# Kernel tuning notes

Hardware: AMD Instinct MI355X
Metric: run time of the kernel (lower is better)

The kernel has to match this reference:

```python
import jax, jax.numpy as jnp
import numpy as np

N_FEAT = 1024
NEG_INF = -1e30  # stand-in for -inf that is safe in fp32 softmax


def setup_inputs() -> dict:
    key = jax.random.key(0)
    k1, k2 = jax.random.split(key)
    T, C = 4096, N_FEAT
    x = jax.random.normal(k1, (T, C), dtype=jnp.float32)
    W = jax.random.normal(k2, (C, 3 * C), dtype=jnp.float32) * (1.0 / np.sqrt(C))
    b = jnp.zeros((3 * C,), dtype=jnp.float32)
    return {"x": x, "W": W, "b": b, "n_padd": 0}


def reference(x, W, b, n_padd):
    T, C = x.shape
    qkv = x @ W + b                      # [T, 3C]
    q, k, v = jnp.split(qkv, 3, axis=1)  # each [T, C]
    att = (q @ k.T) * (1.0 / jnp.sqrt(jnp.float32(C)))  # [T, T]
    idx = jnp.arange(T)
    # causal mask AND padding mask: only keys >= n_padd for queries >= n_padd
    mask = (idx[None, :] <= idx[:, None]) & (idx[None, :] >= n_padd) & (idx[:, None] >= n_padd)
    att = jnp.where(mask, att, NEG_INF)
    att = jax.nn.softmax(att, axis=-1)
    y = att @ v                          # [T, C]
    return y
```

## Files before the change

kernel.cpp:

```cpp
#include <hip/hip_runtime.h>
#include <hip/hip_bf16.h>
#include <math.h>

#define C_DIM 1024
#define QKS  2048

typedef __attribute__((ext_vector_type(8))) short bf16x8;
typedef __attribute__((ext_vector_type(4))) float f32x4;

__device__ __forceinline__ unsigned short f2bf(float f) {
  __hip_bfloat16 h = __float2bfloat16(f);
  return *(reinterpret_cast<unsigned short*>(&h));
}
__device__ __forceinline__ float bf2f(unsigned short u) {
  return __uint_as_float(((unsigned int)u) << 16);
}
__device__ __forceinline__ f32x4 mfma16(bf16x8 a, bf16x8 b, f32x4 c) {
  return __builtin_amdgcn_mfma_f32_16x16x32_bf16(a, b, c, 0, 0, 0);
}
__device__ __forceinline__ void gload_lds16(const unsigned short* g,
                                            unsigned short* l) {
  __builtin_amdgcn_global_load_lds(
      (const __attribute__((address_space(1))) void*)(g),
      (__attribute__((address_space(3))) void*)(l), 16, 0, 0);
}

#define VMCNT(n)  asm volatile("s_waitcnt vmcnt(" #n ")" ::: "memory")
#define LGKMCNT0  asm volatile("s_waitcnt lgkmcnt(0)" ::: "memory")
#define SBAR      __builtin_amdgcn_sched_barrier(0)
#define BARRIER   __builtin_amdgcn_s_barrier()
#define PRIO1     __builtin_amdgcn_s_setprio(1)
#define PRIO0     __builtin_amdgcn_s_setprio(0)

__global__ __launch_bounds__(256) void cast_x(
    const float* __restrict__ x, unsigned short* __restrict__ xb) {
  const int i = (blockIdx.x * 256 + threadIdx.x) << 2;
  float4 v = *(const float4*)(x + i);
  ushort4 u;
  u.x = f2bf(v.x); u.y = f2bf(v.y); u.z = f2bf(v.z); u.w = f2bf(v.w);
  *(ushort4*)(xb + i) = u;
}

__global__ __launch_bounds__(256) void transpose_w(
    const float* __restrict__ W, unsigned short* __restrict__ WT) {
  __shared__ float Ls[64][65];
  const int n0 = blockIdx.x * 64;
  const int k0 = blockIdx.y * 64;
  const int c = (threadIdx.x & 15) << 2;
  const int r = threadIdx.x >> 4;
#pragma unroll
  for (int rr = 0; rr < 64; rr += 16) {
    float4 v = *(const float4*)(W + (size_t)(k0 + r + rr) * 3072 + n0 + c);
    Ls[r + rr][c + 0] = v.x; Ls[r + rr][c + 1] = v.y;
    Ls[r + rr][c + 2] = v.z; Ls[r + rr][c + 3] = v.w;
  }
  __syncthreads();
#pragma unroll
  for (int rr = 0; rr < 64; rr += 16) {
    const int X = r + rr;
    ushort4 u;
    u.x = f2bf(Ls[c + 0][X]); u.y = f2bf(Ls[c + 1][X]);
    u.z = f2bf(Ls[c + 2][X]); u.w = f2bf(Ls[c + 3][X]);
    *(ushort4*)(WT + (size_t)(n0 + X) * C_DIM + k0 + c) = u;
  }
}

template <int MODE>
__global__ __launch_bounds__(256) void gemm128(
    const unsigned short* __restrict__ A_, const unsigned short* __restrict__ BT_,
    void* __restrict__ Cv, const float* __restrict__ bias_,
    int lda, int ldb, int ldc, int T) {
  __shared__ __align__(16) unsigned short As[2][2][64][64];
  __shared__ __align__(16) unsigned short Bs[2][2][64][64];

  const int tid = threadIdx.x, lane = tid & 63, w = tid >> 6;
  const int wr = w >> 1, wc = w & 1;
  const int qd = lane >> 4, n16 = lane & 15;

  const unsigned short* A  = A_;
  const unsigned short* BT = BT_;
  const float* bias = bias_;
  unsigned short* Cb = (unsigned short*)Cv;
  float* Cf = (float*)Cv;
  int ldc_ = ldc;
  int m0, n0, kbeg = 0, kend = C_DIM;
  bool use_atomic = false, rowbias = false;

  if (MODE == 4) {
    const int nQKx = QKS >> 7;
    const int nQK  = (T >> 7) * nQKx;
    int id = (int)blockIdx.x;
    if (id < nQK) {
      m0 = (id / nQKx) << 7; n0 = (id % nQKx) << 7;
    } else {
      id -= nQK;
      const int nVx = T >> 7;
      m0 = (id / nVx) << 7; n0 = (id % nVx) << 7;
      A  = BT_ + (size_t)QKS * C_DIM;
      BT = A_;
      Cb = (unsigned short*)Cv + (size_t)T * QKS;
      bias = bias_ + QKS; rowbias = true; ldc_ = T;
    }
  } else if (MODE == 2) {
    if ((int)blockIdx.x > (int)blockIdx.y) return;
    m0 = (int)blockIdx.y << 7; n0 = (int)blockIdx.x << 7;
  } else {
    const int nnx = C_DIM >> 7;
    int id = (int)blockIdx.x;
    const int nx = id % nnx;
    int s = id / nnx;
    int bi = 0;
    while (s >= ((bi >> 3) + 1)) { s -= (bi >> 3) + 1; ++bi; }
    m0 = bi << 7; n0 = nx << 7;
    kbeg = s << 10;
    const int kfull = (bi + 1) << 7;
    kend = kbeg + 1024 < kfull ? kbeg + 1024 : kfull;
    use_atomic = (kfull > 1024);
  }

  const int NT  = (kend - kbeg) >> 6;
  const int nit = NT >> 1;

  const int l3 = lane >> 3;
  const int su = (((lane & 7) ^ l3) << 3);
  const unsigned short* asrc[2][2];
  const unsigned short* bsrc[2][2];
#pragma unroll
  for (int g = 0; g < 2; ++g)
#pragma unroll
    for (int c = 0; c < 2; ++c) {
      asrc[g][c] = A  + (size_t)(m0 + g * 64 + c * 32 + (w << 3) + l3) * lda + kbeg + su;
      bsrc[g][c] = BT + (size_t)(n0 + g * 64 + c * 32 + (w << 3) + l3) * ldb + kbeg + su;
    }

#define STAGE_A(buf, g, kk) do { \
    gload_lds16(asrc[g][0] + (kk), &As[buf][g][(w << 3)][0]);      \
    gload_lds16(asrc[g][1] + (kk), &As[buf][g][32 + (w << 3)][0]); \
  } while (0)
#define STAGE_B(buf, g, kk) do { \
    gload_lds16(bsrc[g][0] + (kk), &Bs[buf][g][(w << 3)][0]);      \
    gload_lds16(bsrc[g][1] + (kk), &Bs[buf][g][32 + (w << 3)][0]); \
  } while (0)

  const int sw0 = ((qd ^ (n16 & 7)) << 3);
  const int sw1 = (((4 + qd) ^ (n16 & 7)) << 3);

#define READ_A(AA, mh, buf) do { \
  _Pragma("unroll") for (int fm = 0; fm < 2; ++fm) { \
    AA[fm][0] = *(const bf16x8*)&As[buf][wr][(mh) * 32 + fm * 16 + n16][sw0]; \
    AA[fm][1] = *(const bf16x8*)&As[buf][wr][(mh) * 32 + fm * 16 + n16][sw1]; \
  } } while (0)
#define READ_B(BB, nh, buf) do { \
  _Pragma("unroll") for (int fn = 0; fn < 2; ++fn) { \
    BB[fn][0] = *(const bf16x8*)&Bs[buf][wc][(nh) * 32 + fn * 16 + n16][sw0]; \
    BB[fn][1] = *(const bf16x8*)&Bs[buf][wc][(nh) * 32 + fn * 16 + n16][sw1]; \
  } } while (0)

  f32x4 acc[4][4];
#pragma unroll
  for (int i = 0; i < 4; ++i)
#pragma unroll
    for (int j = 0; j < 4; ++j) acc[i][j] = (f32x4){0.f, 0.f, 0.f, 0.f};

#define MFMA_QUAD(mh, nh, AA, BB) do { \
  _Pragma("unroll") for (int fm = 0; fm < 2; ++fm) \
  _Pragma("unroll") for (int fn = 0; fn < 2; ++fn) { \
    acc[(mh) * 2 + fm][(nh) * 2 + fn] = mfma16(AA[fm][0], BB[fn][0], acc[(mh) * 2 + fm][(nh) * 2 + fn]); \
    acc[(mh) * 2 + fm][(nh) * 2 + fn] = mfma16(AA[fm][1], BB[fn][1], acc[(mh) * 2 + fm][(nh) * 2 + fn]); \
  } } while (0)

#define PH_SYNC   SBAR; BARRIER; LGKMCNT0; SBAR
#define PH_CLOSE  SBAR; BARRIER

  STAGE_B(0, 0, 0); STAGE_B(0, 1, 0); STAGE_A(0, 0, 0); STAGE_A(0, 1, 0);
  STAGE_B(1, 0, 64); STAGE_B(1, 1, 64);
  VMCNT(4);
  SBAR; BARRIER;

  bf16x8 a[2][2], b0[2][2], b1[2][2];
  for (int i = 0; i + 1 < nit; ++i) {
    const int t  = i << 1;
    const int k1 = (t + 1) << 6, k2 = (t + 2) << 6, k3 = (t + 3) << 6;
    READ_A(a, 0, 0); READ_B(b0, 0, 0);
    STAGE_A(1, 0, k1);
    PH_SYNC; PRIO1; MFMA_QUAD(0, 0, a, b0); PRIO0; PH_CLOSE;
    READ_B(b1, 1, 0);
    STAGE_A(1, 1, k1);
    PH_SYNC; PRIO1; MFMA_QUAD(0, 1, a, b1); PRIO0; PH_CLOSE;
    READ_A(a, 1, 0);
    STAGE_B(0, 0, k2);
    PH_SYNC; PRIO1; MFMA_QUAD(1, 0, a, b0); PRIO0; PH_CLOSE;
    STAGE_B(0, 1, k2);
    VMCNT(4);
    PH_SYNC; PRIO1; MFMA_QUAD(1, 1, a, b1); PRIO0; PH_CLOSE;
    READ_A(a, 0, 1); READ_B(b0, 0, 1);
    STAGE_A(0, 0, k2);
    PH_SYNC; PRIO1; MFMA_QUAD(0, 0, a, b0); PRIO0; PH_CLOSE;
    READ_B(b1, 1, 1);
    STAGE_A(0, 1, k2);
    PH_SYNC; PRIO1; MFMA_QUAD(0, 1, a, b1); PRIO0; PH_CLOSE;
    READ_A(a, 1, 1);
    STAGE_B(1, 0, k3);
    PH_SYNC; PRIO1; MFMA_QUAD(1, 0, a, b0); PRIO0; PH_CLOSE;
    STAGE_B(1, 1, k3);
    VMCNT(4);
    PH_SYNC; PRIO1; MFMA_QUAD(1, 1, a, b1); PRIO0; PH_CLOSE;
  }
  {
    const int k1 = (NT - 1) << 6;
    READ_A(a, 0, 0); READ_B(b0, 0, 0);
    STAGE_A(1, 0, k1);
    PH_SYNC; PRIO1; MFMA_QUAD(0, 0, a, b0); PRIO0; PH_CLOSE;
    READ_B(b1, 1, 0);
    STAGE_A(1, 1, k1);
    PH_SYNC; PRIO1; MFMA_QUAD(0, 1, a, b1); PRIO0; PH_CLOSE;
    READ_A(a, 1, 0);
    PH_SYNC; PRIO1; MFMA_QUAD(1, 0, a, b0); PRIO0; PH_CLOSE;
    VMCNT(0);
    PH_SYNC; PRIO1; MFMA_QUAD(1, 1, a, b1); PRIO0; PH_CLOSE;
    READ_A(a, 0, 1); READ_B(b0, 0, 1);
    PH_SYNC; PRIO1; MFMA_QUAD(0, 0, a, b0); PRIO0; PH_CLOSE;
    READ_B(b1, 1, 1);
    PH_SYNC; PRIO1; MFMA_QUAD(0, 1, a, b1); PRIO0; PH_CLOSE;
    READ_A(a, 1, 1);
    PH_SYNC; PRIO1; MFMA_QUAD(1, 0, a, b0); PRIO0;
    PRIO1; MFMA_QUAD(1, 1, a, b1); PRIO0;
  }

  if (MODE == 3) {
#pragma unroll
    for (int fm = 0; fm < 4; ++fm)
#pragma unroll
      for (int fn = 0; fn < 4; ++fn) {
        const int col  = n0 + (wc << 6) + (fn << 4) + n16;
        const int rowb = m0 + (wr << 6) + (fm << 4) + (qd << 2);
#pragma unroll
        for (int r = 0; r < 4; ++r) {
          if (use_atomic) atomicAdd(&Cf[(size_t)(rowb + r) * ldc_ + col], acc[fm][fn][r]);
          else            Cf[(size_t)(rowb + r) * ldc_ + col] = acc[fm][fn][r];
        }
      }
  } else {
#pragma unroll
    for (int fm = 0; fm < 4; ++fm)
#pragma unroll
      for (int fn = 0; fn < 4; ++fn) {
        const int col  = n0 + (wc << 6) + (fn << 4) + n16;
        const int rowb = m0 + (wr << 6) + (fm << 4) + (qd << 2);
        const float bc = (MODE == 4 && !rowbias) ? bias[col] : 0.f;
#pragma unroll
        for (int r = 0; r < 4; ++r) {
          float v = acc[fm][fn][r];
          if (MODE == 4) v += rowbias ? bias[rowb + r] : bc;
          if (MODE == 2) v *= 0.03125f;
          Cb[(size_t)(rowb + r) * ldc_ + col] = f2bf(v);
        }
      }
  }
#undef STAGE_A
#undef STAGE_B
#undef READ_A
#undef READ_B
#undef MFMA_QUAD
#undef PH_SYNC
#undef PH_CLOSE
}

__global__ __launch_bounds__(256) void softmax_rows(
    unsigned short* __restrict__ P, const int* __restrict__ np_p, int T) {
  __shared__ float red[8];
  const int i = blockIdx.x;
  const int np = *np_p;
  const int klen = ((i >> 7) + 1) << 7;
  const int tid = threadIdx.x, lane = tid & 63, w = tid >> 6;
  const int j0 = tid << 4;
  unsigned short* rowp = P + (size_t)i * T;
  const bool act = j0 < klen;

  if (i < np) {
    if (act) {
      uint4 z = {0, 0, 0, 0};
      *(uint4*)(rowp + j0) = z;
      *(uint4*)(rowp + j0 + 8) = z;
    }
    return;
  }

  float v[16];
  float mx = -3.0e38f;
  if (act) {
    uint4 u0 = *(const uint4*)(rowp + j0);
    uint4 u1 = *(const uint4*)(rowp + j0 + 8);
    const unsigned int uu[8] = {u0.x, u0.y, u0.z, u0.w, u1.x, u1.y, u1.z, u1.w};
#pragma unroll
    for (int u = 0; u < 8; ++u) {
      v[2 * u]     = bf2f(uu[u] & 0xffff);
      v[2 * u + 1] = bf2f(uu[u] >> 16);
    }
#pragma unroll
    for (int u = 0; u < 16; ++u) {
      const int j = j0 + u;
      if (j > i || j < np) v[u] = -3.0e38f;
      mx = fmaxf(mx, v[u]);
    }
  }
  mx = fmaxf(mx, __shfl_xor(mx, 32));
  mx = fmaxf(mx, __shfl_xor(mx, 16));
  mx = fmaxf(mx, __shfl_xor(mx, 8));
  mx = fmaxf(mx, __shfl_xor(mx, 4));
  mx = fmaxf(mx, __shfl_xor(mx, 2));
  mx = fmaxf(mx, __shfl_xor(mx, 1));
  if (lane == 0) red[w] = mx;
  __syncthreads();
  const float M = fmaxf(fmaxf(red[0], red[1]), fmaxf(red[2], red[3]));

  float sum = 0.f;
  if (act) {
#pragma unroll
    for (int u = 0; u < 16; ++u) {
      const float p = (v[u] > -1.0e30f) ? __expf(v[u] - M) : 0.f;
      v[u] = p;
      sum += p;
    }
  }
  sum += __shfl_xor(sum, 32);
  sum += __shfl_xor(sum, 16);
  sum += __shfl_xor(sum, 8);
  sum += __shfl_xor(sum, 4);
  sum += __shfl_xor(sum, 2);
  sum += __shfl_xor(sum, 1);
  if (lane == 0) red[4 + w] = sum;
  __syncthreads();
  const float inv = 1.0f / (red[4] + red[5] + red[6] + red[7]);

  if (act) {
    unsigned int o[8];
#pragma unroll
    for (int u = 0; u < 8; ++u) {
      const unsigned int lo = f2bf(v[2 * u] * inv);
      const unsigned int hi = f2bf(v[2 * u + 1] * inv);
      o[u] = lo | (hi << 16);
    }
    uint4 s0 = {o[0], o[1], o[2], o[3]};
    uint4 s1 = {o[4], o[5], o[6], o[7]};
    *(uint4*)(rowp + j0) = s0;
    *(uint4*)(rowp + j0 + 8) = s1;
  }
}

__global__ __launch_bounds__(256) void zero_hi(float* __restrict__ out) {
  const size_t i = ((size_t)blockIdx.x * 256 + threadIdx.x) * 4 +
                   (size_t)1024 * C_DIM;
  float4 z = {0.f, 0.f, 0.f, 0.f};
  *(float4*)(out + i) = z;
}

__global__ __launch_bounds__(256) void padfix(
    const unsigned short* __restrict__ vtb, const int* __restrict__ np_p,
    float* __restrict__ out, int T) {
  const int np = *np_p;
  const int row0 = blockIdx.x * 32;
  if (row0 >= np) return;
  const int pc = min(np - row0, 32);
  const int c4 = threadIdx.x << 2;
  float a[4] = {0.f, 0.f, 0.f, 0.f};
#pragma unroll
  for (int c = 0; c < 4; ++c) {
    const unsigned short* vr = vtb + (size_t)(c4 + c) * T;
    for (int j = 0; j < T; j += 8) {
      uint4 v = *(const uint4*)(vr + j);
      a[c] += bf2f(v.x & 0xffff) + bf2f(v.x >> 16) + bf2f(v.y & 0xffff) + bf2f(v.y >> 16)
            + bf2f(v.z & 0xffff) + bf2f(v.z >> 16) + bf2f(v.w & 0xffff) + bf2f(v.w >> 16);
    }
  }
  const float inv = 1.0f / (float)T;
  float4 rv = {a[0] * inv, a[1] * inv, a[2] * inv, a[3] * inv};
  for (int r = 0; r < pc; ++r)
    *(float4*)(out + (size_t)(row0 + r) * C_DIM + c4) = rv;
}

extern "C" void kernel_launch(void* const* d_in, const int* in_sizes, int n_in,
                              void* d_out, int out_size, void* d_ws, size_t ws_size,
                              hipStream_t stream) {
  const float* x    = (const float*)d_in[0];
  const float* W    = (const float*)d_in[1];
  const float* b    = (const float*)d_in[2];
  const int* n_padd = (const int*)d_in[3];
  float* out = (float*)d_out;

  const int T = in_sizes[0] / C_DIM;
  unsigned short* qkb = (unsigned short*)d_ws;
  unsigned short* vtb = qkb + (size_t)T * QKS;
  unsigned short* xb  = vtb + (size_t)C_DIM * T;
  unsigned short* WT  = xb  + (size_t)T * C_DIM;
  unsigned short* P   = xb;

  cast_x<<<(T * C_DIM) / 1024, 256, 0, stream>>>(x, xb);
  transpose_w<<<dim3(48, 16), 256, 0, stream>>>(W, WT);

  {
    const int nQK = (T >> 7) * (QKS >> 7);
    const int nV  = (C_DIM >> 7) * (T >> 7);
    gemm128<4><<<nQK + nV, 256, 0, stream>>>(
        xb, WT, qkb, b, C_DIM, C_DIM, QKS, T);
  }
  gemm128<2><<<dim3(T >> 7, T >> 7), 256, 0, stream>>>(
      qkb, qkb + C_DIM, P, b, QKS, QKS, T, T);
  softmax_rows<<<T, 256, 0, stream>>>(P, n_padd, T);
  zero_hi<<<((T - 1024) * C_DIM) / 1024, 256, 0, stream>>>(out);
  {
    const int nyt = T >> 7;
    int slots = 0;
    for (int bi = 0; bi < nyt; ++bi) slots += (bi >> 3) + 1;
    gemm128<3><<<slots * (C_DIM >> 7), 256, 0, stream>>>(
        P, vtb, out, b, T, T, C_DIM, T);
  }
  padfix<<<T / 32, 256, 0, stream>>>(vtb, n_padd, out, T);
}
```

Before: 237.8 us.

## Store GEMM operands in MFMA fragment layout and load directly without LDS

Operands are repacked into a 16x32 fragment-major layout, so the GEMM kernels load MFMA fragments straight from global memory into registers. This replaces the LDS-staged, barrier-heavy pipeline with a simple double-buffered register loop. The softmax now writes probabilities directly in fragment layout through a 128KB LDS staging tile, and block-id swizzling is added to the projection and PV GEMMs. The cost is extra repack kernels and global loads with no LDS reuse across waves, which raises memory and cache traffic.

New measurement: 316.9 us. +33.3%, slower.

```diff
diff --git a/kernel.cpp b/kernel.cpp
--- a/kernel.cpp
+++ b/kernel.cpp
@@ -18,31 +18,27 @@
 __device__ __forceinline__ f32x4 mfma16(bf16x8 a, bf16x8 b, f32x4 c) {
   return __builtin_amdgcn_mfma_f32_16x16x32_bf16(a, b, c, 0, 0, 0);
 }
-__device__ __forceinline__ void gload_lds16(const unsigned short* g,
-                                            unsigned short* l) {
-  __builtin_amdgcn_global_load_lds(
-      (const __attribute__((address_space(1))) void*)(g),
-      (__attribute__((address_space(3))) void*)(l), 16, 0, 0);
-}
-
-#define VMCNT(n)  asm volatile("s_waitcnt vmcnt(" #n ")" ::: "memory")
-#define LGKMCNT0  asm volatile("s_waitcnt lgkmcnt(0)" ::: "memory")
-#define SBAR      __builtin_amdgcn_sched_barrier(0)
-#define BARRIER   __builtin_amdgcn_s_barrier()
-#define PRIO1     __builtin_amdgcn_s_setprio(1)
-#define PRIO0     __builtin_amdgcn_s_setprio(0)
-
-__global__ __launch_bounds__(256) void cast_x(
-    const float* __restrict__ x, unsigned short* __restrict__ xb) {
-  const int i = (blockIdx.x * 256 + threadIdx.x) << 2;
-  float4 v = *(const float4*)(x + i);
-  ushort4 u;
-  u.x = f2bf(v.x); u.y = f2bf(v.y); u.z = f2bf(v.z); u.w = f2bf(v.w);
-  *(ushort4*)(xb + i) = u;
-}
-
-__global__ __launch_bounds__(256) void transpose_w(
-    const float* __restrict__ W, unsigned short* __restrict__ WT) {
+__device__ __forceinline__ int swz8(int bid, int nwg) {
+  const int cpx = nwg >> 3;
+  return (bid & 7) * cpx + (bid >> 3);
+}
+
+
+__global__ __launch_bounds__(256) void cast_xF(
+    const float* __restrict__ x, unsigned short* __restrict__ xbF) {
+  const int id = blockIdx.x * 4 + (threadIdx.x >> 6);
+  const int tr = id >> 5, tk = id & 31;
+  const int lane = threadIdx.x & 63, n16 = lane & 15, qd = lane >> 4;
+  const float* s = x + (size_t)(tr * 16 + n16) * C_DIM + tk * 32 + qd * 8;
+  float4 v0 = *(const float4*)s, v1 = *(const float4*)(s + 4);
+  unsigned short o[8] = {f2bf(v0.x), f2bf(v0.y), f2bf(v0.z), f2bf(v0.w),
+                         f2bf(v1.x), f2bf(v1.y), f2bf(v1.z), f2bf(v1.w)};
+  *(uint4*)(xbF + (((size_t)tr * 32 + tk) << 9) + ((size_t)lane << 3)) =
+      *(const uint4*)o;
+}
+
+__global__ __launch_bounds__(256) void transpose_wF(
+    const float* __restrict__ W, unsigned short* __restrict__ WTF) {
   __shared__ float Ls[64][65];
   const int n0 = blockIdx.x * 64;
   const int k0 = blockIdx.y * 64;
@@ -56,105 +52,91 @@
   }
   __syncthreads();
 #pragma unroll
-  for (int rr = 0; rr < 64; rr += 16) {
-    const int X = r + rr;
-    ushort4 u;
-    u.x = f2bf(Ls[c + 0][X]); u.y = f2bf(Ls[c + 1][X]);
-    u.z = f2bf(Ls[c + 2][X]); u.w = f2bf(Ls[c + 3][X]);
-    *(ushort4*)(WT + (size_t)(n0 + X) * C_DIM + k0 + c) = u;
-  }
+  for (int it = 0; it < 2; ++it) {
+    const int slot = it * 256 + threadIdx.x;
+    const int l = slot & 63, cell = slot >> 6;
+    const int nb = cell & 3, kb = cell >> 2;
+    const int n16 = l & 15, qd = l >> 4;
+    unsigned short o[8];
+#pragma unroll
+    for (int e = 0; e < 8; ++e)
+      o[e] = f2bf(Ls[kb * 32 + qd * 8 + e][nb * 16 + n16]);
+    *(uint4*)(WTF + ((((size_t)((n0 >> 4) + nb)) * 32 + ((k0 >> 5) + kb)) << 9)
+              + ((size_t)l << 3)) = *(const uint4*)o;
+  }
+}
+
+__global__ __launch_bounds__(256) void repackF(
+    const unsigned short* __restrict__ src, unsigned short* __restrict__ dst,
+    int ldS, int KB) {
+  const int id = blockIdx.x * 4 + (threadIdx.x >> 6);
+  const int tr = id / KB, tk = id % KB;
+  const int lane = threadIdx.x & 63, n16 = lane & 15, qd = lane >> 4;
+  uint4 v = *(const uint4*)(src + (size_t)(tr * 16 + n16) * ldS + tk * 32 + qd * 8);
+  *(uint4*)(dst + (((size_t)tr * KB + tk) << 9) + ((size_t)lane << 3)) = v;
 }
 
 template <int MODE>
-__global__ __launch_bounds__(256) void gemm128(
-    const unsigned short* __restrict__ A_, const unsigned short* __restrict__ BT_,
+__global__ __launch_bounds__(256) void gemmF(
+    const unsigned short* __restrict__ AF, const unsigned short* __restrict__ BF,
     void* __restrict__ Cv, const float* __restrict__ bias_,
-    int lda, int ldb, int ldc, int T) {
-  __shared__ __align__(16) unsigned short As[2][2][64][64];
-  __shared__ __align__(16) unsigned short Bs[2][2][64][64];
-
+    int KB, int ldc, int T) {
   const int tid = threadIdx.x, lane = tid & 63, w = tid >> 6;
   const int wr = w >> 1, wc = w & 1;
   const int qd = lane >> 4, n16 = lane & 15;
 
-  const unsigned short* A  = A_;
-  const unsigned short* BT = BT_;
+  const unsigned short* Ae = AF;
+  const unsigned short* Be = BF;
   const float* bias = bias_;
   unsigned short* Cb = (unsigned short*)Cv;
   float* Cf = (float*)Cv;
   int ldc_ = ldc;
-  int m0, n0, kbeg = 0, kend = C_DIM;
+  int m0, n0, aro, bro, kbeg = 0, kend = C_DIM;
   bool use_atomic = false, rowbias = false;
 
   if (MODE == 4) {
     const int nQKx = QKS >> 7;
     const int nQK  = (T >> 7) * nQKx;
-    int id = (int)blockIdx.x;
+    int id = swz8((int)blockIdx.x, nQK + ((C_DIM >> 7) * (T >> 7)));
     if (id < nQK) {
       m0 = (id / nQKx) << 7; n0 = (id % nQKx) << 7;
+      aro = m0; bro = n0;
     } else {
       id -= nQK;
       const int nVx = T >> 7;
       m0 = (id / nVx) << 7; n0 = (id % nVx) << 7;
-      A  = BT_ + (size_t)QKS * C_DIM;
-      BT = A_;
+      Ae = BF; Be = AF;
+      aro = QKS + m0; bro = n0;
       Cb = (unsigned short*)Cv + (size_t)T * QKS;
       bias = bias_ + QKS; rowbias = true; ldc_ = T;
     }
   } else if (MODE == 2) {
     if ((int)blockIdx.x > (int)blockIdx.y) return;
     m0 = (int)blockIdx.y << 7; n0 = (int)blockIdx.x << 7;
+    aro = m0; bro = n0;
   } else {
     const int nnx = C_DIM >> 7;
-    int id = (int)blockIdx.x;
+    int id = swz8((int)blockIdx.x, (int)gridDim.x);
     const int nx = id % nnx;
     int s = id / nnx;
     int bi = 0;
     while (s >= ((bi >> 3) + 1)) { s -= (bi >> 3) + 1; ++bi; }
     m0 = bi << 7; n0 = nx << 7;
+    aro = m0; bro = n0;
     kbeg = s << 10;
     const int kfull = (bi + 1) << 7;
     kend = kbeg + 1024 < kfull ? kbeg + 1024 : kfull;
     use_atomic = (kfull > 1024);
   }
 
-  const int NT  = (kend - kbeg) >> 6;
-  const int nit = NT >> 1;
-
-  const int l3 = lane >> 3;
-  const int su = (((lane & 7) ^ l3) << 3);
-  const unsigned short* asrc[2][2];
-  const unsigned short* bsrc[2][2];
-#pragma unroll
-  for (int g = 0; g < 2; ++g)
-#pragma unroll
-    for (int c = 0; c < 2; ++c) {
-      asrc[g][c] = A  + (size_t)(m0 + g * 64 + c * 32 + (w << 3) + l3) * lda + kbeg + su;
-      bsrc[g][c] = BT + (size_t)(n0 + g * 64 + c * 32 + (w << 3) + l3) * ldb + kbeg + su;
-    }
-
-#define STAGE_A(buf, g, kk) do { \
-    gload_lds16(asrc[g][0] + (kk), &As[buf][g][(w << 3)][0]);      \
-    gload_lds16(asrc[g][1] + (kk), &As[buf][g][32 + (w << 3)][0]); \
-  } while (0)
-#define STAGE_B(buf, g, kk) do { \
-    gload_lds16(bsrc[g][0] + (kk), &Bs[buf][g][(w << 3)][0]);      \
-    gload_lds16(bsrc[g][1] + (kk), &Bs[buf][g][32 + (w << 3)][0]); \
-  } while (0)
-
-  const int sw0 = ((qd ^ (n16 & 7)) << 3);
-  const int sw1 = (((4 + qd) ^ (n16 & 7)) << 3);
-
-#define READ_A(AA, mh, buf) do { \
-  _Pragma("unroll") for (int fm = 0; fm < 2; ++fm) { \
-    AA[fm][0] = *(const bf16x8*)&As[buf][wr][(mh) * 32 + fm * 16 + n16][sw0]; \
-    AA[fm][1] = *(const bf16x8*)&As[buf][wr][(mh) * 32 + fm * 16 + n16][sw1]; \
-  } } while (0)
-#define READ_B(BB, nh, buf) do { \
-  _Pragma("unroll") for (int fn = 0; fn < 2; ++fn) { \
-    BB[fn][0] = *(const bf16x8*)&Bs[buf][wc][(nh) * 32 + fn * 16 + n16][sw0]; \
-    BB[fn][1] = *(const bf16x8*)&Bs[buf][wc][(nh) * 32 + fn * 16 + n16][sw1]; \
-  } } while (0)
+  const int NS = (kend - kbeg) >> 5;
+  const int kb0 = kbeg >> 5;
+  const size_t fmS = (size_t)KB << 9;
+
+  const unsigned short* ap =
+      Ae + ((((size_t)((aro >> 4) + wr * 4)) * KB + kb0) << 9) + ((size_t)lane << 3);
+  const unsigned short* bp =
+      Be + ((((size_t)((bro >> 4) + wc * 4)) * KB + kb0) << 9) + ((size_t)lane << 3);
 
   f32x4 acc[4][4];
 #pragma unroll
@@ -162,69 +144,40 @@
 #pragma unroll
     for (int j = 0; j < 4; ++j) acc[i][j] = (f32x4){0.f, 0.f, 0.f, 0.f};
 
-#define MFMA_QUAD(mh, nh, AA, BB) do { \
-  _Pragma("unroll") for (int fm = 0; fm < 2; ++fm) \
-  _Pragma("unroll") for (int fn = 0; fn < 2; ++fn) { \
-    acc[(mh) * 2 + fm][(nh) * 2 + fn] = mfma16(AA[fm][0], BB[fn][0], acc[(mh) * 2 + fm][(nh) * 2 + fn]); \
-    acc[(mh) * 2 + fm][(nh) * 2 + fn] = mfma16(AA[fm][1], BB[fn][1], acc[(mh) * 2 + fm][(nh) * 2 + fn]); \
-  } } while (0)
-
-#define PH_SYNC   SBAR; BARRIER; LGKMCNT0; SBAR
-#define PH_CLOSE  SBAR; BARRIER
-
-  STAGE_B(0, 0, 0); STAGE_B(0, 1, 0); STAGE_A(0, 0, 0); STAGE_A(0, 1, 0);
-  STAGE_B(1, 0, 64); STAGE_B(1, 1, 64);
-  VMCNT(4);
-  SBAR; BARRIER;
-
-  bf16x8 a[2][2], b0[2][2], b1[2][2];
-  for (int i = 0; i + 1 < nit; ++i) {
-    const int t  = i << 1;
-    const int k1 = (t + 1) << 6, k2 = (t + 2) << 6, k3 = (t + 3) << 6;
-    READ_A(a, 0, 0); READ_B(b0, 0, 0);
-    STAGE_A(1, 0, k1);
-    PH_SYNC; PRIO1; MFMA_QUAD(0, 0, a, b0); PRIO0; PH_CLOSE;
-    READ_B(b1, 1, 0);
-    STAGE_A(1, 1, k1);
-    PH_SYNC; PRIO1; MFMA_QUAD(0, 1, a, b1); PRIO0; PH_CLOSE;
-    READ_A(a, 1, 0);
-    STAGE_B(0, 0, k2);
-    PH_SYNC; PRIO1; MFMA_QUAD(1, 0, a, b0); PRIO0; PH_CLOSE;
-    STAGE_B(0, 1, k2);
-    VMCNT(4);
-    PH_SYNC; PRIO1; MFMA_QUAD(1, 1, a, b1); PRIO0; PH_CLOSE;
-    READ_A(a, 0, 1); READ_B(b0, 0, 1);
-    STAGE_A(0, 0, k2);
-    PH_SYNC; PRIO1; MFMA_QUAD(0, 0, a, b0); PRIO0; PH_CLOSE;
-    READ_B(b1, 1, 1);
-    STAGE_A(0, 1, k2);
-    PH_SYNC; PRIO1; MFMA_QUAD(0, 1, a, b1); PRIO0; PH_CLOSE;
-    READ_A(a, 1, 1);
-    STAGE_B(1, 0, k3);
-    PH_SYNC; PRIO1; MFMA_QUAD(1, 0, a, b0); PRIO0; PH_CLOSE;
-    STAGE_B(1, 1, k3);
-    VMCNT(4);
-    PH_SYNC; PRIO1; MFMA_QUAD(1, 1, a, b1); PRIO0; PH_CLOSE;
-  }
-  {
-    const int k1 = (NT - 1) << 6;
-    READ_A(a, 0, 0); READ_B(b0, 0, 0);
-    STAGE_A(1, 0, k1);
-    PH_SYNC; PRIO1; MFMA_QUAD(0, 0, a, b0); PRIO0; PH_CLOSE;
-    READ_B(b1, 1, 0);
-    STAGE_A(1, 1, k1);
-    PH_SYNC; PRIO1; MFMA_QUAD(0, 1, a, b1); PRIO0; PH_CLOSE;
-    READ_A(a, 1, 0);
-    PH_SYNC; PRIO1; MFMA_QUAD(1, 0, a, b0); PRIO0; PH_CLOSE;
-    VMCNT(0);
-    PH_SYNC; PRIO1; MFMA_QUAD(1, 1, a, b1); PRIO0; PH_CLOSE;
-    READ_A(a, 0, 1); READ_B(b0, 0, 1);
-    PH_SYNC; PRIO1; MFMA_QUAD(0, 0, a, b0); PRIO0; PH_CLOSE;
-    READ_B(b1, 1, 1);
-    PH_SYNC; PRIO1; MFMA_QUAD(0, 1, a, b1); PRIO0; PH_CLOSE;
-    READ_A(a, 1, 1);
-    PH_SYNC; PRIO1; MFMA_QUAD(1, 0, a, b0); PRIO0;
-    PRIO1; MFMA_QUAD(1, 1, a, b1); PRIO0;
+  bf16x8 aX[4], bX[4], aY[4], bY[4];
+#pragma unroll
+  for (int f = 0; f < 4; ++f) {
+    aX[f] = *(const bf16x8*)(ap + f * fmS);
+    bX[f] = *(const bf16x8*)(bp + f * fmS);
+  }
+
+  for (int t = 0; t < NS; t += 2) {
+    const unsigned short* ap1 = ap + (size_t)(t + 1) * 512;
+    const unsigned short* bp1 = bp + (size_t)(t + 1) * 512;
+#pragma unroll
+    for (int f = 0; f < 4; ++f) {
+      aY[f] = *(const bf16x8*)(ap1 + f * fmS);
+      bY[f] = *(const bf16x8*)(bp1 + f * fmS);
+    }
+#pragma unroll
+    for (int fm = 0; fm < 4; ++fm)
+#pragma unroll
+      for (int fn = 0; fn < 4; ++fn)
+        acc[fm][fn] = mfma16(aX[fm], bX[fn], acc[fm][fn]);
+    if (t + 2 < NS) {
+      const unsigned short* ap2 = ap + (size_t)(t + 2) * 512;
+      const unsigned short* bp2 = bp + (size_t)(t + 2) * 512;
+#pragma unroll
+      for (int f = 0; f < 4; ++f) {
+        aX[f] = *(const bf16x8*)(ap2 + f * fmS);
+        bX[f] = *(const bf16x8*)(bp2 + f * fmS);
+      }
+    }
+#pragma unroll
+    for (int fm = 0; fm < 4; ++fm)
+#pragma unroll
+      for (int fn = 0; fn < 4; ++fn)
+        acc[fm][fn] = mfma16(aY[fm], bY[fn], acc[fm][fn]);
   }
 
   if (MODE == 3) {
@@ -257,94 +210,89 @@
         }
       }
   }
-#undef STAGE_A
-#undef STAGE_B
-#undef READ_A
-#undef READ_B
-#undef MFMA_QUAD
-#undef PH_SYNC
-#undef PH_CLOSE
-}
-
-__global__ __launch_bounds__(256) void softmax_rows(
-    unsigned short* __restrict__ P, const int* __restrict__ np_p, int T) {
-  __shared__ float red[8];
-  const int i = blockIdx.x;
+}
+
+__global__ __launch_bounds__(256) void softmaxF(
+    unsigned short* __restrict__ SP, const int* __restrict__ np_p, int T) {
+  __shared__ unsigned short LT[65536];
   const int np = *np_p;
-  const int klen = ((i >> 7) + 1) << 7;
-  const int tid = threadIdx.x, lane = tid & 63, w = tid >> 6;
-  const int j0 = tid << 4;
-  unsigned short* rowp = P + (size_t)i * T;
-  const bool act = j0 < klen;
-
-  if (i < np) {
-    if (act) {
-      uint4 z = {0, 0, 0, 0};
-      *(uint4*)(rowp + j0) = z;
-      *(uint4*)(rowp + j0 + 8) = z;
-    }
-    return;
-  }
-
-  float v[16];
+  const int sb = blockIdx.x;
+  const int tid = threadIdx.x;
+  const int KB = T >> 5;
+  const int klen = ((sb >> 3) + 1) << 7;
+
+  const int r16 = tid >> 4, c = tid & 15;
+  const int row = sb * 16 + r16;
+  const int run = klen >> 4;
+  const unsigned short* rp = SP + (size_t)row * T + c * run;
+  const int kbase = c * run;
+
   float mx = -3.0e38f;
-  if (act) {
-    uint4 u0 = *(const uint4*)(rowp + j0);
-    uint4 u1 = *(const uint4*)(rowp + j0 + 8);
-    const unsigned int uu[8] = {u0.x, u0.y, u0.z, u0.w, u1.x, u1.y, u1.z, u1.w};
-#pragma unroll
-    for (int u = 0; u < 8; ++u) {
-      v[2 * u]     = bf2f(uu[u] & 0xffff);
-      v[2 * u + 1] = bf2f(uu[u] >> 16);
-    }
-#pragma unroll
-    for (int u = 0; u < 16; ++u) {
-      const int j = j0 + u;
-      if (j > i || j < np) v[u] = -3.0e38f;
-      mx = fmaxf(mx, v[u]);
-    }
-  }
-  mx = fmaxf(mx, __shfl_xor(mx, 32));
-  mx = fmaxf(mx, __shfl_xor(mx, 16));
+  for (int j = 0; j < run; j += 8) {
+    uint4 u = *(const uint4*)(rp + j);
+    const unsigned int uu[4] = {u.x, u.y, u.z, u.w};
+#pragma unroll
+    for (int h = 0; h < 4; ++h) {
+      const int k0e = kbase + j + 2 * h;
+      const float v0 = bf2f(uu[h] & 0xffff), v1 = bf2f(uu[h] >> 16);
+      if (k0e     <= row && k0e     >= np) mx = fmaxf(mx, v0);
+      if (k0e + 1 <= row && k0e + 1 >= np) mx = fmaxf(mx, v1);
+    }
+  }
   mx = fmaxf(mx, __shfl_xor(mx, 8));
   mx = fmaxf(mx, __shfl_xor(mx, 4));
   mx = fmaxf(mx, __shfl_xor(mx, 2));
   mx = fmaxf(mx, __shfl_xor(mx, 1));
-  if (lane == 0) red[w] = mx;
-  __syncthreads();
-  const float M = fmaxf(fmaxf(red[0], red[1]), fmaxf(red[2], red[3]));
 
   float sum = 0.f;
-  if (act) {
-#pragma unroll
-    for (int u = 0; u < 16; ++u) {
-      const float p = (v[u] > -1.0e30f) ? __expf(v[u] - M) : 0.f;
-      v[u] = p;
-      sum += p;
-    }
-  }
-  sum += __shfl_xor(sum, 32);
-  sum += __shfl_xor(sum, 16);
+  for (int j = 0; j < run; j += 8) {
+    uint4 u = *(const uint4*)(rp + j);
+    const unsigned int uu[4] = {u.x, u.y, u.z, u.w};
+#pragma unroll
+    for (int h = 0; h < 4; ++h) {
+      const int k0e = kbase + j + 2 * h;
+      const float v0 = bf2f(uu[h] & 0xffff), v1 = bf2f(uu[h] >> 16);
+      if (k0e     <= row && k0e     >= np) sum += __expf(v0 - mx);
+      if (k0e + 1 <= row && k0e + 1 >= np) sum += __expf(v1 - mx);
+    }
+  }
   sum += __shfl_xor(sum, 8);
   sum += __shfl_xor(sum, 4);
   sum += __shfl_xor(sum, 2);
   sum += __shfl_xor(sum, 1);
-  if (lane == 0) red[4 + w] = sum;
+  const float inv = (sum > 0.f) ? 1.0f / sum : 0.f;
+
+  float* Mf = (float*)LT;
+  if (c == 0) { Mf[r16] = mx; Mf[16 + r16] = inv; }
   __syncthreads();
-  const float inv = 1.0f / (red[4] + red[5] + red[6] + red[7]);
-
-  if (act) {
-    unsigned int o[8];
-#pragma unroll
-    for (int u = 0; u < 8; ++u) {
-      const unsigned int lo = f2bf(v[2 * u] * inv);
-      const unsigned int hi = f2bf(v[2 * u + 1] * inv);
-      o[u] = lo | (hi << 16);
-    }
-    uint4 s0 = {o[0], o[1], o[2], o[3]};
-    uint4 s1 = {o[4], o[5], o[6], o[7]};
-    *(uint4*)(rowp + j0) = s0;
-    *(uint4*)(rowp + j0 + 8) = s1;
+  const int myr = tid & 15;
+  const float M3 = Mf[myr], I3 = Mf[16 + myr];
+  const int row3 = sb * 16 + myr;
+  const bool dead3 = row3 < np;
+  __syncthreads();
+
+  const int nst = klen * 2;
+  for (int s = tid; s < nst; s += 256) {
+    const int kc = (s >> 4) << 3;
+    uint4 u = *(const uint4*)(SP + (size_t)row3 * T + kc);
+    const unsigned int uu[4] = {u.x, u.y, u.z, u.w};
+    unsigned short o[8];
+#pragma unroll
+    for (int h = 0; h < 4; ++h) {
+      const int ke = kc + 2 * h;
+      const float v0 = bf2f(uu[h] & 0xffff), v1 = bf2f(uu[h] >> 16);
+      const float p0 = (!dead3 && ke     <= row3 && ke     >= np) ? __expf(v0 - M3) * I3 : 0.f;
+      const float p1 = (!dead3 && ke + 1 <= row3 && ke + 1 >= np) ? __expf(v1 - M3) * I3 : 0.f;
+      o[2 * h] = f2bf(p0); o[2 * h + 1] = f2bf(p1);
+    }
+    *(uint4*)(LT + (size_t)s * 8) = *(const uint4*)o;
+  }
+  __syncthreads();
+
+  unsigned short* dst = SP + (((size_t)sb * KB) << 9);
+  for (int s = tid; s < nst; s += 256) {
+    uint4 v = *(const uint4*)(LT + (size_t)s * 8);
+    *(uint4*)(dst + (size_t)s * 8) = v;
   }
 }
 
@@ -355,22 +303,25 @@
   *(float4*)(out + i) = z;
 }
 
-__global__ __launch_bounds__(256) void padfix(
-    const unsigned short* __restrict__ vtb, const int* __restrict__ np_p,
+__global__ __launch_bounds__(256) void padfixF(
+    const unsigned short* __restrict__ vF, const int* __restrict__ np_p,
     float* __restrict__ out, int T) {
   const int np = *np_p;
   const int row0 = blockIdx.x * 32;
   if (row0 >= np) return;
   const int pc = min(np - row0, 32);
   const int c4 = threadIdx.x << 2;
+  const int KB = T >> 5;
   float a[4] = {0.f, 0.f, 0.f, 0.f};
 #pragma unroll
-  for (int c = 0; c < 4; ++c) {
-    const unsigned short* vr = vtb + (size_t)(c4 + c) * T;
-    for (int j = 0; j < T; j += 8) {
-      uint4 v = *(const uint4*)(vr + j);
-      a[c] += bf2f(v.x & 0xffff) + bf2f(v.x >> 16) + bf2f(v.y & 0xffff) + bf2f(v.y >> 16)
-            + bf2f(v.z & 0xffff) + bf2f(v.z >> 16) + bf2f(v.w & 0xffff) + bf2f(v.w >> 16);
+  for (int cc = 0; cc < 4; ++cc) {
+    const int ccol = c4 + cc;
+    const unsigned short* base =
+        vF + ((((size_t)(ccol >> 4)) * KB) << 9) + ((size_t)(ccol & 15) << 3);
+    for (int u = 0; u < KB * 4; ++u) {
+      uint4 v = *(const uint4*)(base + ((size_t)u << 7));
+      a[cc] += bf2f(v.x & 0xffff) + bf2f(v.x >> 16) + bf2f(v.y & 0xffff) + bf2f(v.y >> 16)
+             + bf2f(v.z & 0xffff) + bf2f(v.z >> 16) + bf2f(v.w & 0xffff) + bf2f(v.w >> 16);
     }
   }
   const float inv = 1.0f / (float)T;
@@ -389,31 +340,38 @@
   float* out = (float*)d_out;
 
   const int T = in_sizes[0] / C_DIM;
-  unsigned short* qkb = (unsigned short*)d_ws;
-  unsigned short* vtb = qkb + (size_t)T * QKS;
-  unsigned short* xb  = vtb + (size_t)C_DIM * T;
-  unsigned short* WT  = xb  + (size_t)T * C_DIM;
-  unsigned short* P   = xb;
-
-  cast_x<<<(T * C_DIM) / 1024, 256, 0, stream>>>(x, xb);
-  transpose_w<<<dim3(48, 16), 256, 0, stream>>>(W, WT);
+  unsigned short* ws  = (unsigned short*)d_ws;
+  unsigned short* qkb = ws;
+  unsigned short* vtb = ws + (size_t)8388608;
+  unsigned short* xbF = ws + (size_t)12582912;
+  unsigned short* S   = ws;
+  unsigned short* vF  = ws + (size_t)16777216;
+  unsigned short* qF  = ws + (size_t)20971520;
+  unsigned short* WTF = qF;
+  unsigned short* kF  = ws + (size_t)25165824;
+
+  cast_xF<<<2048, 256, 0, stream>>>(x, xbF);
+  transpose_wF<<<dim3(48, 16), 256, 0, stream>>>(W, WTF);
 
   {
     const int nQK = (T >> 7) * (QKS >> 7);
     const int nV  = (C_DIM >> 7) * (T >> 7);
-    gemm128<4><<<nQK + nV, 256, 0, stream>>>(
-        xb, WT, qkb, b, C_DIM, C_DIM, QKS, T);
-  }
-  gemm128<2><<<dim3(T >> 7, T >> 7), 256, 0, stream>>>(
-      qkb, qkb + C_DIM, P, b, QKS, QKS, T, T);
-  softmax_rows<<<T, 256, 0, stream>>>(P, n_padd, T);
+    gemmF<4><<<nQK + nV, 256, 0, stream>>>(
+        xbF, WTF, qkb, b, 32, QKS, T);
+  }
+  repackF<<<2048, 256, 0, stream>>>(qkb,        qF, QKS, 32);
+  repackF<<<2048, 256, 0, stream>>>(qkb + 1024, kF, QKS, 32);
+  repackF<<<2048, 256, 0, stream>>>(vtb,        vF, T,  128);
+  gemmF<2><<<dim3(T >> 7, T >> 7), 256, 0, stream>>>(
+      qF, kF, S, b, 32, T, T);
+  softmaxF<<<T / 16, 256, 0, stream>>>(S, n_padd, T);
   zero_hi<<<((T - 1024) * C_DIM) / 1024, 256, 0, stream>>>(out);
   {
     const int nyt = T >> 7;
     int slots = 0;
     for (int bi = 0; bi < nyt; ++bi) slots += (bi >> 3) + 1;
-    gemm128<3><<<slots * (C_DIM >> 7), 256, 0, stream>>>(
-        P, vtb, out, b, T, T, C_DIM, T);
-  }
-  padfix<<<T / 32, 256, 0, stream>>>(vtb, n_padd, out, T);
-}
+    gemmF<3><<<slots * (C_DIM >> 7), 256, 0, stream>>>(
+        S, vF, out, b, 128, C_DIM, T);
+  }
+  padfixF<<<T / 32, 256, 0, stream>>>(vF, n_padd, out, T);
+}
```
